# Kernel tuning notes

Measured on AMD Instinct MI355X. Metric: run time of the kernel, lower is better.

Reference implementation:

```python
import jax, jax.numpy as jnp
import numpy as np

B, T, C, H, HS, L, V, BITS = 4, 512, 768, 12, 64, 12, 50257, 16


def _ln(x, g, b, eps=1e-5):
    m = x.mean(-1, keepdims=True)
    v = ((x - m) ** 2).mean(-1, keepdims=True)
    return (x - m) * jax.lax.rsqrt(v + eps) * g + b


def setup_inputs() -> dict:
    key = jax.random.key(0)
    ks = jax.random.split(key, 12)
    s = 0.02
    return {
        "idx": jax.random.randint(ks[0], (B, T), 0, V),
        "tok_emb": jax.random.normal(ks[1], (V, C), jnp.float32) * s,
        "pos_emb": jax.random.normal(ks[2], (T, C), jnp.float32) * s,
        "Wq": jax.random.normal(ks[3], (L, H, C, HS), jnp.float32) * s,
        "Wk": jax.random.normal(ks[4], (L, H, C, HS), jnp.float32) * s,
        "Wv": jax.random.normal(ks[5], (L, H, C, HS), jnp.float32) * s,
        "Wo": jax.random.normal(ks[6], (L, C, C), jnp.float32) * s,
        "bo": jnp.zeros((L, C), jnp.float32),
        "W1": jax.random.normal(ks[7], (L, C, 4 * C), jnp.float32) * s,
        "b1": jnp.zeros((L, 4 * C), jnp.float32),
        "W2": jax.random.normal(ks[8], (L, 4 * C, C), jnp.float32) * s,
        "b2": jnp.zeros((L, C), jnp.float32),
        "ln1_g": jnp.ones((L, C), jnp.float32),
        "ln1_b": jnp.zeros((L, C), jnp.float32),
        "ln2_g": jnp.ones((L, C), jnp.float32),
        "ln2_b": jnp.zeros((L, C), jnp.float32),
        "lnf_g": jnp.ones((C,), jnp.float32),
        "lnf_b": jnp.zeros((C,), jnp.float32),
        "Wh": jax.random.normal(ks[9], (C, BITS), jnp.float32) * s,
        "bh": jnp.zeros((BITS,), jnp.float32),
    }


def reference(idx, tok_emb, pos_emb, Wq, Wk, Wv, Wo, bo, W1, b1, W2, b2,
              ln1_g, ln1_b, ln2_g, ln2_b, lnf_g, lnf_b, Wh, bh):
    Bc, Tc = idx.shape
    x = tok_emb[idx] + pos_emb[:Tc]          # [B,T,C]
    mask = jnp.tril(jnp.ones((Tc, Tc), bool))  # causal tril buffer
    scale = HS ** -0.5

    def block(x, p):
        wq, wk, wv, wo, bo_, w1, b1_, w2, b2_, g1, bb1, g2, bb2 = p
        xn = _ln(x, g1, bb1)
        q = jnp.einsum('btc,hcd->bhtd', xn, wq)
        k = jnp.einsum('btc,hcd->bhtd', xn, wk)
        v = jnp.einsum('btc,hcd->bhtd', xn, wv)
        wei = jnp.einsum('bhtd,bhsd->bhts', q, k) * scale
        wei = jnp.where(mask, wei, -jnp.inf)
        wei = jax.nn.softmax(wei, axis=-1)
        o = jnp.einsum('bhts,bhsd->bhtd', wei, v)
        o = o.transpose(0, 2, 1, 3).reshape(Bc, Tc, H * HS)  # concat heads
        x = x + o @ wo + bo_
        xn2 = _ln(x, g2, bb2)
        h = jax.nn.gelu(xn2 @ w1 + b1_, approximate=False)  # exact GELU (torch default)
        x = x + h @ w2 + b2_
        return x, None

    x, _ = jax.lax.scan(block, x, (Wq, Wk, Wv, Wo, bo, W1, b1, W2, b2,
                                   ln1_g, ln1_b, ln2_g, ln2_b))
    x = _ln(x, lnf_g, lnf_b)
    logits = x @ Wh + bh                      # [B,T,16] ECOC logits
    return logits
```

## Files before the change

kernel.cpp:

```cpp
#include <hip/hip_runtime.h>
#include <hip/hip_bf16.h>
#include <math.h>

#define TT   512
#define CC   768
#define HH   12
#define HSZ  64
#define LL   12
#define C4   3072
#define BTOT 2048
#define NQKV 2304
#define NX   ((long)BTOT * CC)

typedef __attribute__((ext_vector_type(8))) short short8;
typedef __attribute__((ext_vector_type(4))) float f32x4;

__device__ __forceinline__ unsigned short f2b_bits(float f) {
    unsigned u = __float_as_uint(f);
    return (unsigned short)((u + 0x7fffu + ((u >> 16) & 1u)) >> 16);
}

__device__ __forceinline__ void gl_lds16(const void* g, void* l) {
    __builtin_amdgcn_global_load_lds(
        (const __attribute__((address_space(1))) unsigned int*)g,
        (__attribute__((address_space(3))) unsigned int*)l,
        16, 0, 0);
}

__global__ __launch_bounds__(256) void embed_k(const int* __restrict__ idx,
    const float* __restrict__ tok, const float* __restrict__ pos,
    float* __restrict__ x)
{
    int r   = blockIdx.x;
    int tid = threadIdx.x;
    int t   = r & (TT - 1);
    long id = idx[r];
    const float* te = tok + id * (long)CC;
    const float* pe = pos + (long)t * CC;
    float* xr = x + (long)r * CC;
#pragma unroll
    for (int i = 0; i < 3; ++i) {
        int c = tid + i * 256;
        xr[c] = te[c] + pe[c];
    }
}

__global__ __launch_bounds__(256) void ln_b(const float* __restrict__ x,
    const float* __restrict__ g, const float* __restrict__ b,
    __hip_bfloat16* __restrict__ y)
{
    int r = blockIdx.x, tid = threadIdx.x;
    const float* xr = x + (long)r * CC;
    float v[3];
    v[0] = xr[tid]; v[1] = xr[tid + 256]; v[2] = xr[tid + 512];
    float s  = v[0] + v[1] + v[2];
    float sq = v[0]*v[0] + v[1]*v[1] + v[2]*v[2];
#pragma unroll
    for (int off = 32; off > 0; off >>= 1) {
        s  += __shfl_down(s, off);
        sq += __shfl_down(sq, off);
    }
    __shared__ float ss[4], ssq[4];
    int w = tid >> 6;
    if ((tid & 63) == 0) { ss[w] = s; ssq[w] = sq; }
    __syncthreads();
    s  = ss[0] + ss[1] + ss[2] + ss[3];
    sq = ssq[0] + ssq[1] + ssq[2] + ssq[3];
    float mean = s * (1.0f / CC);
    float var  = sq * (1.0f / CC) - mean * mean;
    float rs   = rsqrtf(var + 1e-5f);
    __hip_bfloat16* yr = y + (long)r * CC;
#pragma unroll
    for (int i = 0; i < 3; ++i) {
        int c = tid + i * 256;
        yr[c] = __float2bfloat16((v[i] - mean) * rs * g[c] + b[c]);
    }
}

template <bool DOLN>
__global__ __launch_bounds__(256) void red_ln(float* __restrict__ x,
    const float* __restrict__ p, const float* __restrict__ bias,
    const float* __restrict__ g, const float* __restrict__ b,
    __hip_bfloat16* __restrict__ y)
{
    int r = blockIdx.x, tid = threadIdx.x;
    float* xr = x + (long)r * CC;
    const float* pr = p + (long)r * CC;
    float v[3];
#pragma unroll
    for (int i = 0; i < 3; ++i) {
        int c = tid + i * 256;
        float s = xr[c] + bias[c];
        s += pr[c];
        s += pr[c + 1 * NX];
        s += pr[c + 2 * NX];
        s += pr[c + 3 * NX];
        xr[c] = s;
        v[i] = s;
    }
    if (!DOLN) return;
    float s  = v[0] + v[1] + v[2];
    float sq = v[0]*v[0] + v[1]*v[1] + v[2]*v[2];
#pragma unroll
    for (int off = 32; off > 0; off >>= 1) {
        s  += __shfl_down(s, off);
        sq += __shfl_down(sq, off);
    }
    __shared__ float ss[4], ssq[4];
    int w = tid >> 6;
    if ((tid & 63) == 0) { ss[w] = s; ssq[w] = sq; }
    __syncthreads();
    s  = ss[0] + ss[1] + ss[2] + ss[3];
    sq = ssq[0] + ssq[1] + ssq[2] + ssq[3];
    float mean = s * (1.0f / CC);
    float var  = sq * (1.0f / CC) - mean * mean;
    float rs   = rsqrtf(var + 1e-5f);
    __hip_bfloat16* yr = y + (long)r * CC;
#pragma unroll
    for (int i = 0; i < 3; ++i) {
        int c = tid + i * 256;
        yr[c] = __float2bfloat16((v[i] - mean) * rs * g[c] + b[c]);
    }
}

__global__ __launch_bounds__(256) void cvtT_k(const float* __restrict__ src,
    __hip_bfloat16* __restrict__ dst, int R, int D, long sSrc, long sDst)
{
    src += (long)blockIdx.z * sSrc;
    dst += (long)blockIdx.z * sDst;
    __shared__ float t[64][65];
    int d0 = blockIdx.x * 64, r0 = blockIdx.y * 64;
    int tid = threadIdx.x;
#pragma unroll
    for (int i = 0; i < 4; ++i) {
        int flat = tid + i * 256;
        int r = flat >> 4, c4 = (flat & 15) * 4;
        float4 v = *(const float4*)&src[(long)(r0 + r) * D + d0 + c4];
        t[r][c4 + 0] = v.x; t[r][c4 + 1] = v.y;
        t[r][c4 + 2] = v.z; t[r][c4 + 3] = v.w;
    }
    __syncthreads();
#pragma unroll
    for (int i = 0; i < 4; ++i) {
        int flat = tid + i * 256;
        int n = flat >> 4, kq = (flat & 15) * 4;
        ushort4 o;
        o.x = f2b_bits(t[kq + 0][n]); o.y = f2b_bits(t[kq + 1][n]);
        o.z = f2b_bits(t[kq + 2][n]); o.w = f2b_bits(t[kq + 3][n]);
        *(ushort4*)&dst[(long)(d0 + n) * R + r0 + kq] = o;
    }
}

__global__ __launch_bounds__(256) void cvt_qkvT(const float* __restrict__ Wq,
    const float* __restrict__ Wk, const float* __restrict__ Wv,
    __hip_bfloat16* __restrict__ out)
{
    int c0 = blockIdx.x * 64;
    int g  = blockIdx.y;
    int l  = blockIdx.z;
    int which = g / 12, h = g % 12;
    const long wAtt = (long)HH * CC * HSZ;
    const float* src = (which == 0 ? Wq : which == 1 ? Wk : Wv)
                       + l * wAtt + (long)h * CC * HSZ;
    __hip_bfloat16* dst = out + (long)l * NQKV * CC + (long)(which * CC + h * HSZ) * CC;
    __shared__ float t[64][65];
    int tid = threadIdx.x;
#pragma unroll
    for (int i = 0; i < 4; ++i) {
        int flat = tid + i * 256;
        int r = flat >> 4, c4 = (flat & 15) * 4;
        float4 v = *(const float4*)&src[(long)(c0 + r) * HSZ + c4];
        t[r][c4 + 0] = v.x; t[r][c4 + 1] = v.y;
        t[r][c4 + 2] = v.z; t[r][c4 + 3] = v.w;
    }
    __syncthreads();
#pragma unroll
    for (int i = 0; i < 4; ++i) {
        int flat = tid + i * 256;
        int n = flat >> 4, kq = (flat & 15) * 4;
        ushort4 o;
        o.x = f2b_bits(t[kq + 0][n]); o.y = f2b_bits(t[kq + 1][n]);
        o.z = f2b_bits(t[kq + 2][n]); o.w = f2b_bits(t[kq + 3][n]);
        *(ushort4*)&dst[(long)n * CC + c0 + kq] = o;
    }
}

template <int EPI>
__global__ __launch_bounds__(256, 3) void gemm_bf16(
    const __hip_bfloat16* __restrict__ A,
    const __hip_bfloat16* __restrict__ BT,
    __hip_bfloat16* __restrict__ Cb, float* __restrict__ Cf,
    const float* __restrict__ bias, __hip_bfloat16* __restrict__ Vt,
    int K, int lda, int ldb, int ldc)
{
    __shared__ short Asm[4][64 * 32];
    __shared__ short Bsm[4][128 * 32];
    const int tid  = threadIdx.x;
    const int lane = tid & 63;
    const int wid  = tid >> 6;
    const int wm = wid >> 1, wn = wid & 1;

    const int gx = gridDim.x;
    const int slice = gx * gridDim.y;
    int flat = blockIdx.y * gx + blockIdx.x;
    int swz  = (flat & 7) * (slice >> 3) + (flat >> 3);
    const int row0 = (swz / gx) * 64, col0 = (swz % gx) * 128;
    const int sk = (EPI == 5) ? blockIdx.z : 0;

    const int gr = tid >> 2;
    const int cb = ((tid & 3) + (tid >> 3)) & 3;
    const int gk = cb * 8;
    const __hip_bfloat16* Ap = A  + (long)(row0 + gr) * lda + sk * K + gk;
    const __hip_bfloat16* Bp = BT + (long)(col0 + gr) * ldb + sk * K + gk;
    const int lofs = wid * 512;

    f32x4 acc[2][4] = {};
    const int fr = lane & 15, g = lane >> 4;

    int offA[2], offB[4];
#pragma unroll
    for (int m = 0; m < 2; ++m) {
        int row = wm * 32 + m * 16 + fr;
        offA[m] = row * 32 + (((g - (row >> 1)) & 3) * 8);
    }
#pragma unroll
    for (int n = 0; n < 4; ++n) {
        int row = wn * 64 + n * 16 + fr;
        offB[n] = row * 32 + (((g - (row >> 1)) & 3) * 8);
    }

#define STAGE(buf)                                                          \
    do {                                                                    \
        gl_lds16(Ap, &Asm[buf][lofs]);                                      \
        gl_lds16(Bp, &Bsm[buf][lofs]);                                      \
        gl_lds16(Bp + (long)64 * ldb, &Bsm[buf][lofs + 64 * 32]);           \
        Ap += 32; Bp += 32;                                                 \
    } while (0)

    STAGE(0); STAGE(1); STAGE(2);

    const int nt = K >> 5;
    for (int t = 0; t < nt; ++t) {
        if (t < nt - 2)       asm volatile("s_waitcnt vmcnt(6)" ::: "memory");
        else if (t == nt - 2) asm volatile("s_waitcnt vmcnt(3)" ::: "memory");
        else                  asm volatile("s_waitcnt vmcnt(0)" ::: "memory");
        __builtin_amdgcn_s_barrier();
        __builtin_amdgcn_sched_barrier(0);
        if (t + 3 < nt) STAGE((t + 3) & 3);

        const int cur = t & 3;
        short8 af[2], bf[4];
#pragma unroll
        for (int m = 0; m < 2; ++m)
            af[m] = *(const short8*)&Asm[cur][offA[m]];
#pragma unroll
        for (int n = 0; n < 4; ++n)
            bf[n] = *(const short8*)&Bsm[cur][offB[n]];
#pragma unroll
        for (int m = 0; m < 2; ++m)
#pragma unroll
            for (int n = 0; n < 4; ++n)
                acc[m][n] = __builtin_amdgcn_mfma_f32_16x16x32_bf16(
                    af[m], bf[n], acc[m][n], 0, 0, 0);
    }
#undef STAGE

    const int fq = lane >> 4;
    float* pout = (EPI == 5) ? (Cf + (long)sk * NX) : nullptr;
#pragma unroll
    for (int m = 0; m < 2; ++m) {
        int rbase = row0 + wm * 32 + m * 16 + fq * 4;
#pragma unroll
        for (int n = 0; n < 4; ++n) {
            int col = col0 + wn * 64 + n * 16 + fr;
            if (EPI == 1 && col >= 1536) {
                int hd = col - 1536;
                int b = rbase >> 9, t = rbase & (TT - 1);
                ushort4 o;
                o.x = f2b_bits(acc[m][n][0]); o.y = f2b_bits(acc[m][n][1]);
                o.z = f2b_bits(acc[m][n][2]); o.w = f2b_bits(acc[m][n][3]);
                *(ushort4*)&Vt[((long)(b * HH + (hd >> 6)) * HSZ + (hd & 63)) * TT + t] = o;
                continue;
            }
            float bv = (EPI == 2) ? bias[col] : 0.f;
#pragma unroll
            for (int j = 0; j < 4; ++j) {
                long row = rbase + j;
                float v = acc[m][n][j];
                if (EPI == 1) {
                    Cb[row * ldc + col] = __float2bfloat16(v);
                } else if (EPI == 2) {
                    v += bv;
                    v = 0.5f * v * (1.0f + erff(v * 0.70710678118654752f));
                    Cb[row * ldc + col] = __float2bfloat16(v);
                } else {
                    pout[row * ldc + col] = v;
                }
            }
        }
    }
}

__global__ __launch_bounds__(64) void attn_mfma(
    const __hip_bfloat16* __restrict__ qkv,
    const __hip_bfloat16* __restrict__ vT,
    __hip_bfloat16* __restrict__ o)
{
    int flat = blockIdx.x + 32 * (blockIdx.y + 12 * blockIdx.z);
    int swz  = (flat & 7) * 192 + (flat >> 3);
    const int qt = swz & 31;
    const int h  = (swz >> 5) % 12;
    const int b  = swz / 384;
    const int lane = threadIdx.x;
    const int t0 = qt * 16;
    const int fr = lane & 15, g = lane >> 4;

    __shared__ unsigned short P_lds[16 * 40];
    __shared__ float corr_lds[16], l_lds[16];

    const long qbase = ((long)(b * TT + t0 + fr)) * NQKV + h * HSZ + g * 8;
    short8 qf0 = *(const short8*)(qkv + qbase);
    short8 qf1 = *(const short8*)(qkv + qbase + 32);

    f32x4 oacc[4] = {};
    float m_run = -3.0e38f, l_run = 0.f;
    const int t_lane = t0 + fr;
    const int smax = t0 + 15;
    const long kcol = CC + h * HSZ + g * 8;
    const long vrow = (((long)(b * HH + h) * HSZ) + fr) * TT + g * 8;

    short8 ka0, ka1, ka2, ka3;
    {
        long kb0 = ((long)(b * TT + fr)) * NQKV + kcol;
        long kb1 = ((long)(b * TT + 16 + fr)) * NQKV + kcol;
        ka0 = *(const short8*)(qkv + kb0);
        ka1 = *(const short8*)(qkv + kb0 + 32);
        ka2 = *(const short8*)(qkv + kb1);
        ka3 = *(const short8*)(qkv + kb1 + 32);
    }

    for (int s0 = 0; s0 <= smax; s0 += 32) {
        f32x4 st0 = {}, st1 = {};
        st0 = __builtin_amdgcn_mfma_f32_16x16x32_bf16(ka0, qf0, st0, 0, 0, 0);
        st0 = __builtin_amdgcn_mfma_f32_16x16x32_bf16(ka1, qf1, st0, 0, 0, 0);
        st1 = __builtin_amdgcn_mfma_f32_16x16x32_bf16(ka2, qf0, st1, 0, 0, 0);
        st1 = __builtin_amdgcn_mfma_f32_16x16x32_bf16(ka3, qf1, st1, 0, 0, 0);

        const bool more = (s0 + 32 <= smax);
        short8 kn0, kn1, kn2, kn3;
        if (more) {
            long kb0 = ((long)(b * TT + s0 + 32 + fr)) * NQKV + kcol;
            long kb1 = ((long)(b * TT + s0 + 48 + fr)) * NQKV + kcol;
            kn0 = *(const short8*)(qkv + kb0);
            kn1 = *(const short8*)(qkv + kb0 + 32);
            kn2 = *(const short8*)(qkv + kb1);
            kn3 = *(const short8*)(qkv + kb1 + 32);
        }
        short8 vc0 = *(const short8*)(vT + vrow + s0);
        short8 vc1 = *(const short8*)(vT + vrow + 16 * TT + s0);
        short8 vc2 = *(const short8*)(vT + vrow + 32 * TT + s0);
        short8 vc3 = *(const short8*)(vT + vrow + 48 * TT + s0);

        float p[8];
        float mx = -3.0e38f;
#pragma unroll
        for (int j = 0; j < 4; ++j) {
            int s = s0 + g * 4 + j;
            float v = st0[j] * 0.125f;
            v = (s <= t_lane) ? v : -3.0e38f;
            p[j] = v; mx = fmaxf(mx, v);
        }
#pragma unroll
        for (int j = 0; j < 4; ++j) {
            int s = s0 + 16 + g * 4 + j;
            float v = st1[j] * 0.125f;
            v = (s <= t_lane) ? v : -3.0e38f;
            p[4 + j] = v; mx = fmaxf(mx, v);
        }
        mx = fmaxf(mx, __shfl_xor(mx, 16));
        mx = fmaxf(mx, __shfl_xor(mx, 32));
        float mnew = fmaxf(m_run, mx);
        float corr = __expf(m_run - mnew);
        float psum = 0.f;
#pragma unroll
        for (int i = 0; i < 8; ++i) {
            float e = __expf(p[i] - mnew);
            p[i] = e; psum += e;
        }
        psum += __shfl_xor(psum, 16);
        psum += __shfl_xor(psum, 32);
        l_run = l_run * corr + psum;
        m_run = mnew;

        __syncthreads();
        if (lane < 16) corr_lds[lane] = corr;
        unsigned u0 = (unsigned)f2b_bits(p[0]) | ((unsigned)f2b_bits(p[1]) << 16);
        unsigned u1 = (unsigned)f2b_bits(p[2]) | ((unsigned)f2b_bits(p[3]) << 16);
        unsigned u2 = (unsigned)f2b_bits(p[4]) | ((unsigned)f2b_bits(p[5]) << 16);
        unsigned u3 = (unsigned)f2b_bits(p[6]) | ((unsigned)f2b_bits(p[7]) << 16);
        *(unsigned*)&P_lds[fr * 40 + g * 4]          = u0;
        *(unsigned*)&P_lds[fr * 40 + g * 4 + 2]      = u1;
        *(unsigned*)&P_lds[fr * 40 + 16 + g * 4]     = u2;
        *(unsigned*)&P_lds[fr * 40 + 16 + g * 4 + 2] = u3;
        __syncthreads();

        float cr0 = corr_lds[g * 4 + 0], cr1 = corr_lds[g * 4 + 1];
        float cr2 = corr_lds[g * 4 + 2], cr3 = corr_lds[g * 4 + 3];
        short8 pf = *(const short8*)&P_lds[fr * 40 + g * 8];
        oacc[0][0] *= cr0; oacc[0][1] *= cr1; oacc[0][2] *= cr2; oacc[0][3] *= cr3;
        oacc[0] = __builtin_amdgcn_mfma_f32_16x16x32_bf16(pf, vc0, oacc[0], 0, 0, 0);
        oacc[1][0] *= cr0; oacc[1][1] *= cr1; oacc[1][2] *= cr2; oacc[1][3] *= cr3;
        oacc[1] = __builtin_amdgcn_mfma_f32_16x16x32_bf16(pf, vc1, oacc[1], 0, 0, 0);
        oacc[2][0] *= cr0; oacc[2][1] *= cr1; oacc[2][2] *= cr2; oacc[2][3] *= cr3;
        oacc[2] = __builtin_amdgcn_mfma_f32_16x16x32_bf16(pf, vc2, oacc[2], 0, 0, 0);
        oacc[3][0] *= cr0; oacc[3][1] *= cr1; oacc[3][2] *= cr2; oacc[3][3] *= cr3;
        oacc[3] = __builtin_amdgcn_mfma_f32_16x16x32_bf16(pf, vc3, oacc[3], 0, 0, 0);

        if (more) { ka0 = kn0; ka1 = kn1; ka2 = kn2; ka3 = kn3; }
    }

    __syncthreads();
    if (lane < 16) l_lds[lane] = l_run;
    __syncthreads();
    float il0 = 1.f / l_lds[g * 4 + 0], il1 = 1.f / l_lds[g * 4 + 1];
    float il2 = 1.f / l_lds[g * 4 + 2], il3 = 1.f / l_lds[g * 4 + 3];
#pragma unroll
    for (int dt = 0; dt < 4; ++dt) {
        long cbase = (long)(b * TT + t0) * CC + h * HSZ + dt * 16 + fr;
        o[cbase + (g * 4 + 0) * (long)CC] = __float2bfloat16(oacc[dt][0] * il0);
        o[cbase + (g * 4 + 1) * (long)CC] = __float2bfloat16(oacc[dt][1] * il1);
        o[cbase + (g * 4 + 2) * (long)CC] = __float2bfloat16(oacc[dt][2] * il2);
        o[cbase + (g * 4 + 3) * (long)CC] = __float2bfloat16(oacc[dt][3] * il3);
    }
}

__global__ __launch_bounds__(256) void head_k(const float* __restrict__ x,
    const float* __restrict__ g, const float* __restrict__ bb,
    const float* __restrict__ Wh, const float* __restrict__ bh,
    float* __restrict__ out)
{
    int r = blockIdx.x, tid = threadIdx.x;
    const float* xr = x + (long)r * CC;
    float v[3];
    v[0] = xr[tid]; v[1] = xr[tid + 256]; v[2] = xr[tid + 512];
    float s  = v[0] + v[1] + v[2];
    float sq = v[0]*v[0] + v[1]*v[1] + v[2]*v[2];
#pragma unroll
    for (int off = 32; off > 0; off >>= 1) {
        s  += __shfl_down(s, off);
        sq += __shfl_down(sq, off);
    }
    __shared__ float ss[4], ssq[4];
    int w = tid >> 6;
    if ((tid & 63) == 0) { ss[w] = s; ssq[w] = sq; }
    __syncthreads();
    s  = ss[0] + ss[1] + ss[2] + ss[3];
    sq = ssq[0] + ssq[1] + ssq[2] + ssq[3];
    float mean = s * (1.0f / CC);
    float var  = sq * (1.0f / CC) - mean * mean;
    float rs   = rsqrtf(var + 1e-5f);

    float acc[16];
#pragma unroll
    for (int j = 0; j < 16; ++j) acc[j] = 0.f;
#pragma unroll
    for (int i = 0; i < 3; ++i) {
        int c = tid + i * 256;
        float xnv = (v[i] - mean) * rs * g[c] + bb[c];
        const float* wr = Wh + (long)c * 16;
#pragma unroll
        for (int j = 0; j < 16; ++j) acc[j] = fmaf(xnv, wr[j], acc[j]);
    }
#pragma unroll
    for (int off = 32; off > 0; off >>= 1)
#pragma unroll
        for (int j = 0; j < 16; ++j) acc[j] += __shfl_down(acc[j], off);
    __shared__ float red[4][16];
    if ((tid & 63) == 0)
#pragma unroll
        for (int j = 0; j < 16; ++j) red[w][j] = acc[j];
    __syncthreads();
    if (tid < 16)
        out[(long)r * 16 + tid] =
            red[0][tid] + red[1][tid] + red[2][tid] + red[3][tid] + bh[tid];
}

extern "C" void kernel_launch(void* const* d_in, const int* in_sizes, int n_in,
                              void* d_out, int out_size, void* d_ws, size_t ws_size,
                              hipStream_t stream)
{
    const int*   idx  = (const int*)  d_in[0];
    const float* tok  = (const float*)d_in[1];
    const float* pos  = (const float*)d_in[2];
    const float* Wq   = (const float*)d_in[3];
    const float* Wk   = (const float*)d_in[4];
    const float* Wv   = (const float*)d_in[5];
    const float* Wo   = (const float*)d_in[6];
    const float* bo   = (const float*)d_in[7];
    const float* W1   = (const float*)d_in[8];
    const float* b1   = (const float*)d_in[9];
    const float* W2   = (const float*)d_in[10];
    const float* b2   = (const float*)d_in[11];
    const float* ln1g = (const float*)d_in[12];
    const float* ln1b = (const float*)d_in[13];
    const float* ln2g = (const float*)d_in[14];
    const float* ln2b = (const float*)d_in[15];
    const float* lnfg = (const float*)d_in[16];
    const float* lnfb = (const float*)d_in[17];
    const float* Wh   = (const float*)d_in[18];
    const float* bh   = (const float*)d_in[19];

    char* w = (char*)d_ws;
    float*          x     = (float*)w;          w += NX * 4;
    __hip_bfloat16* xn_b  = (__hip_bfloat16*)w; w += NX * 2;
    __hip_bfloat16* qkvb  = (__hip_bfloat16*)w; w += (long)BTOT * NQKV * 2;
    __hip_bfloat16* vT    = (__hip_bfloat16*)w; w += NX * 2;
    __hip_bfloat16* o_b   = (__hip_bfloat16*)w; w += NX * 2;
    __hip_bfloat16* hb    = (__hip_bfloat16*)w; w += (long)BTOT * C4 * 2;
    __hip_bfloat16* qkvT  = (__hip_bfloat16*)w; w += (long)LL * NQKV * CC * 2;
    __hip_bfloat16* woT   = (__hip_bfloat16*)w; w += (long)LL * CC * CC * 2;
    __hip_bfloat16* w1T   = (__hip_bfloat16*)w; w += (long)LL * C4 * CC * 2;
    __hip_bfloat16* w2T   = (__hip_bfloat16*)w; w += (long)LL * CC * C4 * 2;
    float*          pbuf  = (float*)w;          w += 4 * NX * 4;

    cvt_qkvT<<<dim3(12, 36, LL), 256, 0, stream>>>(Wq, Wk, Wv, qkvT);
    cvtT_k<<<dim3(12, 12, LL), 256, 0, stream>>>(Wo, woT, CC, CC,
        (long)CC * CC, (long)CC * CC);
    cvtT_k<<<dim3(48, 12, LL), 256, 0, stream>>>(W1, w1T, CC, C4,
        (long)CC * C4, (long)CC * C4);
    cvtT_k<<<dim3(12, 48, LL), 256, 0, stream>>>(W2, w2T, C4, CC,
        (long)C4 * CC, (long)C4 * CC);

    embed_k<<<BTOT, 256, 0, stream>>>(idx, tok, pos, x);
    ln_b<<<BTOT, 256, 0, stream>>>(x, ln1g, ln1b, xn_b);

    for (int l = 0; l < LL; ++l) {
        gemm_bf16<1><<<dim3(NQKV / 128, BTOT / 64), 256, 0, stream>>>(
            xn_b, qkvT + (long)l * NQKV * CC, qkvb, nullptr, nullptr, vT,
            CC, CC, CC, NQKV);

        attn_mfma<<<dim3(TT / 16, HH, 4), 64, 0, stream>>>(qkvb, vT, o_b);

        gemm_bf16<5><<<dim3(CC / 128, BTOT / 64, 4), 256, 0, stream>>>(
            o_b, woT + (long)l * CC * CC, nullptr, pbuf, nullptr, nullptr,
            192, CC, CC, CC);

        red_ln<true><<<BTOT, 256, 0, stream>>>(x, pbuf, bo + l * CC,
            ln2g + l * CC, ln2b + l * CC, xn_b);

        gemm_bf16<2><<<dim3(C4 / 128, BTOT / 64), 256, 0, stream>>>(
            xn_b, w1T + (long)l * C4 * CC, hb, nullptr, b1 + l * C4, nullptr,
            CC, CC, CC, C4);

        gemm_bf16<5><<<dim3(CC / 128, BTOT / 64, 4), 256, 0, stream>>>(
            hb, w2T + (long)l * CC * C4, nullptr, pbuf, nullptr, nullptr,
            768, C4, C4, CC);

        if (l < LL - 1) {
            red_ln<true><<<BTOT, 256, 0, stream>>>(x, pbuf, b2 + l * CC,
                ln1g + (l + 1) * CC, ln1b + (l + 1) * CC, xn_b);
        } else {
            red_ln<false><<<BTOT, 256, 0, stream>>>(x, pbuf, b2 + l * CC,
                nullptr, nullptr, nullptr);
        }
    }

    head_k<<<BTOT, 256, 0, stream>>>(x, lnfg, lnfb, Wh, bh, (float*)d_out);
}
```

Baseline: 1.504 ms.

## Store split-K partials in bf16 and drop attention block barriers

The split-K partial sums from the Wo and W2 GEMMs are now written as bf16 instead of fp32, and the residual/LN reduction kernel reads them as bf16. This halves the traffic to and from the partial buffer. Separately, the single-wavefront attention kernel replaces its __syncthreads calls with sched_barriers, on the reasoning that one 64-lane wave needs no workgroup barrier. Rounding each partial to bf16 before the reduction adds numerical error to the residual stream.

```diff
diff --git a/kernel.cpp b/kernel.cpp
--- a/kernel.cpp
+++ b/kernel.cpp
@@ -18,6 +18,9 @@
 __device__ __forceinline__ unsigned short f2b_bits(float f) {
     unsigned u = __float_as_uint(f);
     return (unsigned short)((u + 0x7fffu + ((u >> 16) & 1u)) >> 16);
+}
+__device__ __forceinline__ float b2f(unsigned short b) {
+    return __uint_as_float((unsigned)b << 16);
 }
 
 __device__ __forceinline__ void gl_lds16(const void* g, void* l) {
@@ -79,22 +82,22 @@
 
 template <bool DOLN>
 __global__ __launch_bounds__(256) void red_ln(float* __restrict__ x,
-    const float* __restrict__ p, const float* __restrict__ bias,
+    const unsigned short* __restrict__ p, const float* __restrict__ bias,
     const float* __restrict__ g, const float* __restrict__ b,
     __hip_bfloat16* __restrict__ y)
 {
     int r = blockIdx.x, tid = threadIdx.x;
     float* xr = x + (long)r * CC;
-    const float* pr = p + (long)r * CC;
+    const unsigned short* pr = p + (long)r * CC;
     float v[3];
 #pragma unroll
     for (int i = 0; i < 3; ++i) {
         int c = tid + i * 256;
         float s = xr[c] + bias[c];
-        s += pr[c];
-        s += pr[c + 1 * NX];
-        s += pr[c + 2 * NX];
-        s += pr[c + 3 * NX];
+        s += b2f(pr[c]);
+        s += b2f(pr[c + 1 * NX]);
+        s += b2f(pr[c + 2 * NX]);
+        s += b2f(pr[c + 3 * NX]);
         xr[c] = s;
         v[i] = s;
     }
@@ -266,7 +269,6 @@
 #undef STAGE
 
     const int fq = lane >> 4;
-    float* pout = (EPI == 5) ? (Cf + (long)sk * NX) : nullptr;
 #pragma unroll
     for (int m = 0; m < 2; ++m) {
         int rbase = row0 + wm * 32 + m * 16 + fq * 4;
@@ -294,7 +296,7 @@
                     v = 0.5f * v * (1.0f + erff(v * 0.70710678118654752f));
                     Cb[row * ldc + col] = __float2bfloat16(v);
                 } else {
-                    pout[row * ldc + col] = v;
+                    Cb[(long)sk * NX + row * ldc + col] = __float2bfloat16(v);
                 }
             }
         }
@@ -392,7 +394,6 @@
         l_run = l_run * corr + psum;
         m_run = mnew;
 
-        __syncthreads();
         if (lane < 16) corr_lds[lane] = corr;
         unsigned u0 = (unsigned)f2b_bits(p[0]) | ((unsigned)f2b_bits(p[1]) << 16);
         unsigned u1 = (unsigned)f2b_bits(p[2]) | ((unsigned)f2b_bits(p[3]) << 16);
@@ -402,7 +403,7 @@
         *(unsigned*)&P_lds[fr * 40 + g * 4 + 2]      = u1;
         *(unsigned*)&P_lds[fr * 40 + 16 + g * 4]     = u2;
         *(unsigned*)&P_lds[fr * 40 + 16 + g * 4 + 2] = u3;
-        __syncthreads();
+        __builtin_amdgcn_sched_barrier(0);
 
         float cr0 = corr_lds[g * 4 + 0], cr1 = corr_lds[g * 4 + 1];
         float cr2 = corr_lds[g * 4 + 2], cr3 = corr_lds[g * 4 + 3];
@@ -417,11 +418,11 @@
         oacc[3] = __builtin_amdgcn_mfma_f32_16x16x32_bf16(pf, vc3, oacc[3], 0, 0, 0);
 
         if (more) { ka0 = kn0; ka1 = kn1; ka2 = kn2; ka3 = kn3; }
-    }
-
-    __syncthreads();
+        __builtin_amdgcn_sched_barrier(0);
+    }
+
     if (lane < 16) l_lds[lane] = l_run;
-    __syncthreads();
+    __builtin_amdgcn_sched_barrier(0);
     float il0 = 1.f / l_lds[g * 4 + 0], il1 = 1.f / l_lds[g * 4 + 1];
     float il2 = 1.f / l_lds[g * 4 + 2], il3 = 1.f / l_lds[g * 4 + 3];
 #pragma unroll
@@ -521,7 +522,7 @@
     __hip_bfloat16* woT   = (__hip_bfloat16*)w; w += (long)LL * CC * CC * 2;
     __hip_bfloat16* w1T   = (__hip_bfloat16*)w; w += (long)LL * C4 * CC * 2;
     __hip_bfloat16* w2T   = (__hip_bfloat16*)w; w += (long)LL * CC * C4 * 2;
-    float*          pbuf  = (float*)w;          w += 4 * NX * 4;
+    __hip_bfloat16* pbuf  = (__hip_bfloat16*)w; w += 4 * NX * 2;
 
     cvt_qkvT<<<dim3(12, 36, LL), 256, 0, stream>>>(Wq, Wk, Wv, qkvT);
     cvtT_k<<<dim3(12, 12, LL), 256, 0, stream>>>(Wo, woT, CC, CC,
@@ -542,26 +543,26 @@
         attn_mfma<<<dim3(TT / 16, HH, 4), 64, 0, stream>>>(qkvb, vT, o_b);
 
         gemm_bf16<5><<<dim3(CC / 128, BTOT / 64, 4), 256, 0, stream>>>(
-            o_b, woT + (long)l * CC * CC, nullptr, pbuf, nullptr, nullptr,
+            o_b, woT + (long)l * CC * CC, pbuf, nullptr, nullptr, nullptr,
             192, CC, CC, CC);
 
-        red_ln<true><<<BTOT, 256, 0, stream>>>(x, pbuf, bo + l * CC,
-            ln2g + l * CC, ln2b + l * CC, xn_b);
+        red_ln<true><<<BTOT, 256, 0, stream>>>(x, (const unsigned short*)pbuf,
+            bo + l * CC, ln2g + l * CC, ln2b + l * CC, xn_b);
 
         gemm_bf16<2><<<dim3(C4 / 128, BTOT / 64), 256, 0, stream>>>(
             xn_b, w1T + (long)l * C4 * CC, hb, nullptr, b1 + l * C4, nullptr,
             CC, CC, CC, C4);
 
         gemm_bf16<5><<<dim3(CC / 128, BTOT / 64, 4), 256, 0, stream>>>(
-            hb, w2T + (long)l * CC * C4, nullptr, pbuf, nullptr, nullptr,
+            hb, w2T + (long)l * CC * C4, pbuf, nullptr, nullptr, nullptr,
             768, C4, C4, CC);
 
         if (l < LL - 1) {
-            red_ln<true><<<BTOT, 256, 0, stream>>>(x, pbuf, b2 + l * CC,
-                ln1g + (l + 1) * CC, ln1b + (l + 1) * CC, xn_b);
+            red_ln<true><<<BTOT, 256, 0, stream>>>(x, (const unsigned short*)pbuf,
+                b2 + l * CC, ln1g + (l + 1) * CC, ln1b + (l + 1) * CC, xn_b);
         } else {
-            red_ln<false><<<BTOT, 256, 0, stream>>>(x, pbuf, b2 + l * CC,
-                nullptr, nullptr, nullptr);
+            red_ln<false><<<BTOT, 256, 0, stream>>>(x, (const unsigned short*)pbuf,
+                b2 + l * CC, nullptr, nullptr, nullptr);
         }
     }
 
```

Result: faster. 1.447 ms (-3.8%).
